# Performance work log

Measured on AMD Instinct MI355X. Metric: run time of the kernel, lower is better.

Reference implementation:

```python
import jax, jax.numpy as jnp
import numpy as np

N = 20000
NEG_SLOPE = 0.2
BN_EPS = 1e-5


def gat_layer(x, src, dst, W, a_src, a_dst, bias, heads, out_c, concat):
    # x: [N, in_c]; projection to [N, H, C]
    h = (x @ W).reshape(N, heads, out_c)
    al_s = jnp.einsum('nhc,hc->nh', h, a_src)   # per-node source logits
    al_d = jnp.einsum('nhc,hc->nh', h, a_dst)   # per-node dest logits
    e = al_s[src] + al_d[dst]                   # [E, H]
    e = jnp.where(e > 0, e, NEG_SLOPE * e)      # leaky_relu
    # segment softmax over incoming edges of each destination node
    emax = jax.ops.segment_max(e, dst, num_segments=N)
    ee = jnp.exp(e - emax[dst])
    denom = jax.ops.segment_sum(ee, dst, num_segments=N)
    alpha = ee / denom[dst]                     # [E, H]
    msg = h[src] * alpha[:, :, None]            # [E, H, C]
    out = jax.ops.segment_sum(msg, dst, num_segments=N)  # [N, H, C]
    out = out.reshape(N, heads * out_c) if concat else out.mean(axis=1)
    return out + bias


def batchnorm(x, gamma, beta):
    mu = x.mean(axis=0)
    var = x.var(axis=0)
    return (x - mu) * jax.lax.rsqrt(var + BN_EPS) * gamma + beta


def setup_inputs() -> dict:
    key = jax.random.key(0)
    ks = jax.random.split(key, 16)
    E = 320000
    in_c, hid, out_c, H = 128, 32, 16, 8

    def xavier(k, fan_in, fan_out):
        lim = np.sqrt(6.0 / (fan_in + fan_out))
        return jax.random.uniform(k, (fan_in, fan_out), jnp.float32, -lim, lim)

    x = jax.random.normal(ks[0], (N, in_c), jnp.float32)
    edge_index = jax.random.randint(ks[1], (2, E), 0, N, jnp.int32)
    d = {
        'x': x, 'edge_index': edge_index,
        'W0': xavier(ks[2], in_c, hid * H),
        'as0': jax.random.normal(ks[3], (H, hid), jnp.float32) * 0.1,
        'ad0': jax.random.normal(ks[4], (H, hid), jnp.float32) * 0.1,
        'b0': jnp.zeros((hid * H,), jnp.float32),
        'g0': jnp.ones((hid * H,), jnp.float32),
        'be0': jnp.zeros((hid * H,), jnp.float32),
        'W1': xavier(ks[5], hid * H, hid * H),
        'as1': jax.random.normal(ks[6], (H, hid), jnp.float32) * 0.1,
        'ad1': jax.random.normal(ks[7], (H, hid), jnp.float32) * 0.1,
        'b1': jnp.zeros((hid * H,), jnp.float32),
        'g1': jnp.ones((hid * H,), jnp.float32),
        'be1': jnp.zeros((hid * H,), jnp.float32),
        'W2': xavier(ks[8], hid * H, out_c),
        'as2': jax.random.normal(ks[9], (1, out_c), jnp.float32) * 0.1,
        'ad2': jax.random.normal(ks[10], (1, out_c), jnp.float32) * 0.1,
        'b2': jnp.zeros((out_c,), jnp.float32),
    }
    return d


def reference(x, edge_index, W0, as0, ad0, b0, g0, be0,
              W1, as1, ad1, b1, g1, be1, W2, as2, ad2, b2):
    # add self-loops (PyG GATConv default)
    loop = jnp.arange(N, dtype=edge_index.dtype)
    src = jnp.concatenate([edge_index[0], loop])
    dst = jnp.concatenate([edge_index[1], loop])

    h = gat_layer(x, src, dst, W0, as0, ad0, b0, heads=8, out_c=32, concat=True)
    h = jax.nn.relu(batchnorm(h, g0, be0))  # dropout inactive (eval)
    h = gat_layer(h, src, dst, W1, as1, ad1, b1, heads=8, out_c=32, concat=True)
    h = jax.nn.relu(batchnorm(h, g1, be1))
    h = gat_layer(h, src, dst, W2, as2, ad2, b2, heads=1, out_c=16, concat=False)
    return jax.nn.log_softmax(h, axis=-1)
```

## Files before the change

kernel.cpp:

```cpp
#include <hip/hip_runtime.h>
#include <hip/hip_bf16.h>
#include <math.h>


#define LRELU(v) ((v) > 0.f ? (v) : 0.2f * (v))
#define MAXDEG 128

typedef __attribute__((ext_vector_type(8))) short short8v;
typedef __attribute__((ext_vector_type(4))) float f32x4;

__device__ __forceinline__ unsigned short f2b(float f) {
    unsigned u = __float_as_uint(f);
    unsigned r = (u + 0x7fffu + ((u >> 16) & 1u)) >> 16;
    return (unsigned short)r;
}
__device__ __forceinline__ float bl(unsigned u) { return __uint_as_float(u << 16); }
__device__ __forceinline__ float bh(unsigned u) { return __uint_as_float(u & 0xffff0000u); }
__device__ __forceinline__ float b2f(unsigned short u) {
    return __uint_as_float((unsigned)u << 16);
}
__device__ __forceinline__ unsigned pack2(float a, float b) {
    return (unsigned)f2b(a) | ((unsigned)f2b(b) << 16);
}

__device__ __forceinline__ void cvt_body(const float* __restrict__ W,
                                         unsigned short* __restrict__ Wt,
                                         int IN, int OUT, int bx, int by,
                                         float* t ) {
    int tx = threadIdx.x & 31, ty = threadIdx.x >> 5;
    int c0 = bx * 32;
    int r0 = by * 32;
#pragma unroll
    for (int j = 0; j < 32; j += 8)
        t[(ty + j) * 33 + tx] = W[(size_t)(r0 + ty + j) * OUT + c0 + tx];
    __syncthreads();
#pragma unroll
    for (int j = 0; j < 32; j += 8)
        Wt[(size_t)(c0 + ty + j) * IN + r0 + tx] = f2b(t[tx * 33 + ty + j]);
}

__global__ void fill_cvt_k(unsigned* __restrict__ zp, int nz, int gF,
                           const float* __restrict__ W0,
                           unsigned short* __restrict__ Wt0,
                           const float* __restrict__ W1,
                           unsigned short* __restrict__ Wt1) {
    __shared__ float t[32 * 33];
    int b = blockIdx.x;
    if (b < gF) {
        int i = b * 256 + threadIdx.x;
        if (i < nz) zp[i] = 0u;
    } else {
        b -= gF;
        if (b < 32) cvt_body(W0, Wt0, 128, 256, b & 7, b >> 3, t);
        else { b -= 32; cvt_body(W1, Wt1, 256, 256, b & 7, b >> 3, t); }
    }
}

template <int IN, int MODE>
__device__ __forceinline__ void gemm_body(
        const void* __restrict__ Xv,
        const unsigned short* __restrict__ Wt,
        const float* __restrict__ as, const float* __restrict__ ad,
        unsigned short* __restrict__ Y,
        float* __restrict__ als, float* __restrict__ ald, int M,
        int bx, int by, unsigned short* Xs, unsigned short* Ws) {
    constexpr int LDT = 72;
    const int tid = threadIdx.x;
    const int lane = tid & 63, wid = tid >> 6;
    const int wr = wid >> 1, wc = wid & 1;
    const int cl = lane & 15, kg = lane >> 4;
    const int row0 = bx * 64, col0 = by * 64;
    const int sr = tid >> 3;
    const int sk = (tid & 7) * 8;

    f32x4 acc[2][2] = {};

    for (int k0 = 0; k0 < IN; k0 += 64) {
        uint4 xu0 = {0, 0, 0, 0}, xu1 = {0, 0, 0, 0};
        int xr0 = row0 + sr, xr1 = row0 + sr + 32;
        if (MODE == 0) {
            const float* Xf = (const float*)Xv;
            if (xr0 < M) {
                const float* p = Xf + (size_t)xr0 * IN + k0 + sk;
                float4 a = *(const float4*)p, b = *(const float4*)(p + 4);
                xu0 = make_uint4(pack2(a.x, a.y), pack2(a.z, a.w),
                                 pack2(b.x, b.y), pack2(b.z, b.w));
            }
            if (xr1 < M) {
                const float* p = Xf + (size_t)xr1 * IN + k0 + sk;
                float4 a = *(const float4*)p, b = *(const float4*)(p + 4);
                xu1 = make_uint4(pack2(a.x, a.y), pack2(a.z, a.w),
                                 pack2(b.x, b.y), pack2(b.z, b.w));
            }
        } else {
            const unsigned short* Xb = (const unsigned short*)Xv;
            if (xr0 < M) xu0 = *(const uint4*)&Xb[(size_t)xr0 * IN + k0 + sk];
            if (xr1 < M) xu1 = *(const uint4*)&Xb[(size_t)xr1 * IN + k0 + sk];
        }
        uint4 wv0 = *(const uint4*)&Wt[(size_t)(col0 + sr) * IN + k0 + sk];
        uint4 wv1 = *(const uint4*)&Wt[(size_t)(col0 + sr + 32) * IN + k0 + sk];
        __syncthreads();
        *(uint4*)&Xs[sr * LDT + sk] = xu0;
        *(uint4*)&Xs[(sr + 32) * LDT + sk] = xu1;
        *(uint4*)&Ws[sr * LDT + sk] = wv0;
        *(uint4*)&Ws[(sr + 32) * LDT + sk] = wv1;
        __syncthreads();
#pragma unroll
        for (int kk = 0; kk < 64; kk += 32) {
            const int ko = kk + kg * 8;
            short8v a0 = *(const short8v*)&Xs[(wr * 32 + cl) * LDT + ko];
            short8v a1 = *(const short8v*)&Xs[(wr * 32 + 16 + cl) * LDT + ko];
            short8v b0 = *(const short8v*)&Ws[(wc * 32 + cl) * LDT + ko];
            short8v b1 = *(const short8v*)&Ws[(wc * 32 + 16 + cl) * LDT + ko];
            acc[0][0] = __builtin_amdgcn_mfma_f32_16x16x32_bf16(a0, b0, acc[0][0], 0, 0, 0);
            acc[0][1] = __builtin_amdgcn_mfma_f32_16x16x32_bf16(a0, b1, acc[0][1], 0, 0, 0);
            acc[1][0] = __builtin_amdgcn_mfma_f32_16x16x32_bf16(a1, b0, acc[1][0], 0, 0, 0);
            acc[1][1] = __builtin_amdgcn_mfma_f32_16x16x32_bf16(a1, b1, acc[1][1], 0, 0, 0);
        }
    }

#pragma unroll
    for (int mt = 0; mt < 2; mt++)
#pragma unroll
        for (int j = 0; j < 4; j++) {
            int r = row0 + wr * 32 + mt * 16 + kg * 4 + j;
            if (r < M) {
#pragma unroll
                for (int nt = 0; nt < 2; nt++)
                    Y[(size_t)r * 256 + col0 + wc * 32 + nt * 16 + cl] =
                        f2b(acc[mt][nt][j]);
            }
        }

    const int h = 2 * by + wc;
    float as0v = as[h * 32 + cl], as1v = as[h * 32 + 16 + cl];
    float ad0v = ad[h * 32 + cl], ad1v = ad[h * 32 + 16 + cl];
#pragma unroll
    for (int mt = 0; mt < 2; mt++)
#pragma unroll
        for (int j = 0; j < 4; j++) {
            float ps = acc[mt][0][j] * as0v + acc[mt][1][j] * as1v;
            float pd = acc[mt][0][j] * ad0v + acc[mt][1][j] * ad1v;
            ps += __shfl_xor(ps, 1); ps += __shfl_xor(ps, 2);
            ps += __shfl_xor(ps, 4); ps += __shfl_xor(ps, 8);
            pd += __shfl_xor(pd, 1); pd += __shfl_xor(pd, 2);
            pd += __shfl_xor(pd, 4); pd += __shfl_xor(pd, 8);
            int r = row0 + wr * 32 + mt * 16 + kg * 4 + j;
            if (cl == 0 && r < M) {
                als[r * 8 + h] = ps;
                ald[r * 8 + h] = pd;
            }
        }
}

__global__ __launch_bounds__(256) void scatter_gemm0_k(
        const int* __restrict__ ei, int E, int N, int gE,
        int* __restrict__ cnt, int* __restrict__ ssrc,
        const float* __restrict__ x, const unsigned short* __restrict__ Wt0,
        const float* __restrict__ as0, const float* __restrict__ ad0,
        unsigned short* __restrict__ Y,
        float* __restrict__ als, float* __restrict__ ald) {
    __shared__ unsigned short Xs[64 * 72];
    __shared__ unsigned short Ws[64 * 72];
    int b = blockIdx.x;
    if (b < gE) {
        int e = b * 256 + threadIdx.x;
        if (e >= E + N) return;
        int s, d;
        if (e < E) { s = ei[e]; d = ei[E + e]; }
        else       { s = d = e - E; }
        int pos = atomicAdd(&cnt[d], 1);
        if (pos < MAXDEG) ssrc[(size_t)d * MAXDEG + pos] = s;
    } else {
        b -= gE;
        gemm_body<128, 0>(x, Wt0, as0, ad0, Y, als, ald, N, b >> 2, b & 3,
                          Xs, Ws);
    }
}

__global__ __launch_bounds__(256) void gemm_mfma1_k(
        const unsigned short* __restrict__ Xb,
        const unsigned short* __restrict__ Wt,
        const float* __restrict__ as, const float* __restrict__ ad,
        unsigned short* __restrict__ Y,
        float* __restrict__ als, float* __restrict__ ald, int M) {
    __shared__ unsigned short Xs[64 * 72];
    __shared__ unsigned short Ws[64 * 72];
    gemm_body<256, 1>(Xb, Wt, as, ad, Y, als, ald, M,
                      blockIdx.x, blockIdx.y, Xs, Ws);
}

template <int IN>
__global__ void gemm16_k(const unsigned short* __restrict__ X,
                         const float* __restrict__ W,
                         const float* __restrict__ as, const float* __restrict__ ad,
                         float* __restrict__ Y,
                         float* __restrict__ als, float* __restrict__ ald, int M) {
    constexpr int ROWS = 32, OUT = 16, RPT = 2;
    __shared__ float xs[ROWS][IN];
    const int row0 = blockIdx.x * ROWS;
    const int tid = threadIdx.x;
    for (int idx = tid; idx < ROWS * IN; idx += 256) {
        int r = idx / IN, k = idx % IN;
        int gr = row0 + r;
        xs[r][k] = (gr < M) ? b2f(X[(size_t)gr * IN + k]) : 0.f;
    }
    __syncthreads();
    const int j = tid & 15;
    const int rbase = (tid >> 4) * RPT;
    float acc[RPT] = {};
    for (int k = 0; k < IN; k++) {
        float w = W[k * OUT + j];
#pragma unroll
        for (int r = 0; r < RPT; r++) acc[r] += xs[rbase + r][k] * w;
    }
    float a1 = as[j], d1 = ad[j];
#pragma unroll
    for (int r = 0; r < RPT; r++) {
        int gr = row0 + rbase + r;
        if (gr < M) Y[gr * OUT + j] = acc[r];
        float ps = acc[r] * a1, pd = acc[r] * d1;
#pragma unroll
        for (int off = 8; off; off >>= 1) {
            ps += __shfl_xor(ps, off, 16);
            pd += __shfl_xor(pd, off, 16);
        }
        if (j == 0 && gr < M) { als[gr] = ps; ald[gr] = pd; }
    }
}

__global__ void agg8_csr_k(const int* __restrict__ cnt,
                           const int* __restrict__ ssrc,
                           const float* __restrict__ als,
                           const float* __restrict__ ald,
                           const unsigned short* __restrict__ feat,
                           const float* __restrict__ bias,
                           unsigned short* __restrict__ aggb, int N) {
    int lane = threadIdx.x & 63;
    int n = blockIdx.x * 4 + (threadIdx.x >> 6);
    if (n >= N) return;
    int len = cnt[n];
    if (len > MAXDEG) len = MAXDEG;
    const size_t base = (size_t)n * MAXDEG;
    const int grp = lane >> 4;
    const int l = lane & 15;
    const int h = l >> 1;
    const int c0 = l * 16;
    const float adh = ald[n * 8 + h];

    float acc[16] = {};
    float den = 0.f;
    for (int e = grp; e < len; e += 4) {
        int s = ssrc[base + e];
        float v = als[s * 8 + h] + adh;
        v = LRELU(v);
        float p = __expf(v);
        den += p;
        const unsigned short* fp = feat + (size_t)s * 256 + c0;
        uint4 f0 = *(const uint4*)fp;
        uint4 f1 = *(const uint4*)(fp + 8);
        acc[0]  += bl(f0.x) * p; acc[1]  += bh(f0.x) * p;
        acc[2]  += bl(f0.y) * p; acc[3]  += bh(f0.y) * p;
        acc[4]  += bl(f0.z) * p; acc[5]  += bh(f0.z) * p;
        acc[6]  += bl(f0.w) * p; acc[7]  += bh(f0.w) * p;
        acc[8]  += bl(f1.x) * p; acc[9]  += bh(f1.x) * p;
        acc[10] += bl(f1.y) * p; acc[11] += bh(f1.y) * p;
        acc[12] += bl(f1.z) * p; acc[13] += bh(f1.z) * p;
        acc[14] += bl(f1.w) * p; acc[15] += bh(f1.w) * p;
    }
    den += __shfl_xor(den, 16); den += __shfl_xor(den, 32);
#pragma unroll
    for (int j = 0; j < 16; j++) {
        acc[j] += __shfl_xor(acc[j], 16);
        acc[j] += __shfl_xor(acc[j], 32);
    }
    if (lane < 16) {
        float inv = 1.f / den;
        float4 ba = *(const float4*)(bias + c0);
        float4 bb = *(const float4*)(bias + c0 + 4);
        float4 bc = *(const float4*)(bias + c0 + 8);
        float4 bd = *(const float4*)(bias + c0 + 12);
        uint4 o0, o1;
        o0.x = pack2(acc[0]  * inv + ba.x, acc[1]  * inv + ba.y);
        o0.y = pack2(acc[2]  * inv + ba.z, acc[3]  * inv + ba.w);
        o0.z = pack2(acc[4]  * inv + bb.x, acc[5]  * inv + bb.y);
        o0.w = pack2(acc[6]  * inv + bb.z, acc[7]  * inv + bb.w);
        o1.x = pack2(acc[8]  * inv + bc.x, acc[9]  * inv + bc.y);
        o1.y = pack2(acc[10] * inv + bc.z, acc[11] * inv + bc.w);
        o1.z = pack2(acc[12] * inv + bd.x, acc[13] * inv + bd.y);
        o1.w = pack2(acc[14] * inv + bd.z, acc[15] * inv + bd.w);
        unsigned short* op = aggb + (size_t)n * 256 + c0;
        *(uint4*)op = o0;
        *(uint4*)(op + 8) = o1;
    }
}

__global__ void agg1_ls_k(const int* __restrict__ cnt,
                          const int* __restrict__ ssrc,
                          const float* __restrict__ als,
                          const float* __restrict__ ald,
                          const float* __restrict__ feat,
                          const float* __restrict__ b2,
                          float* __restrict__ out, int N) {
    int lane = threadIdx.x & 63;
    int n = blockIdx.x * 4 + (threadIdx.x >> 6);
    if (n >= N) return;
    int len = cnt[n];
    if (len > MAXDEG) len = MAXDEG;
    const size_t base = (size_t)n * MAXDEG;
    float adh = ald[n];

    int slot = lane >> 4, c = lane & 15;
    float acc = 0.f, den = 0.f;
    for (int e = slot; e < len; e += 4) {
        int s = ssrc[base + e];
        float v = als[s] + adh;
        v = LRELU(v);
        float p = __expf(v);
        den += p;
        acc += feat[s * 16 + c] * p;
    }
    acc += __shfl_xor(acc, 16); acc += __shfl_xor(acc, 32);
    den += __shfl_xor(den, 16); den += __shfl_xor(den, 32);

    float v = acc / den + b2[c];
    float mm = v;
#pragma unroll
    for (int off = 8; off; off >>= 1) mm = fmaxf(mm, __shfl_xor(mm, off, 16));
    float ex = __expf(v - mm);
    float ssum = ex;
#pragma unroll
    for (int off = 8; off; off >>= 1) ssum += __shfl_xor(ssum, off, 16);
    if (lane < 16) out[n * 16 + c] = v - mm - logf(ssum);
}

__global__ void bn_stats_k(const unsigned short* __restrict__ agg,
                           float* __restrict__ stats, int N) {
    __shared__ float red[2][8][256];
    const int t = threadIdx.x;
    const int ch0 = (t & 31) * 8;
    const int rslot = t >> 5;
    const int chunk = (N + 63) >> 6;
    const int r0 = blockIdx.x * chunk;
    int r1 = r0 + chunk; if (r1 > N) r1 = N;
    float s[8] = {}, q[8] = {};
    for (int r = r0 + rslot; r < r1; r += 8) {
        uint4 u = *(const uint4*)(agg + (size_t)r * 256 + ch0);
        float v;
        v = bl(u.x); s[0] += v; q[0] += v * v;
        v = bh(u.x); s[1] += v; q[1] += v * v;
        v = bl(u.y); s[2] += v; q[2] += v * v;
        v = bh(u.y); s[3] += v; q[3] += v * v;
        v = bl(u.z); s[4] += v; q[4] += v * v;
        v = bh(u.z); s[5] += v; q[5] += v * v;
        v = bl(u.w); s[6] += v; q[6] += v * v;
        v = bh(u.w); s[7] += v; q[7] += v * v;
    }
#pragma unroll
    for (int j = 0; j < 8; j++) {
        red[0][rslot][ch0 + j] = s[j];
        red[1][rslot][ch0 + j] = q[j];
    }
    __syncthreads();
    float ss = 0.f, qq = 0.f;
#pragma unroll
    for (int k = 0; k < 8; k++) {
        ss += red[0][k][t];
        qq += red[1][k][t];
    }
    atomicAdd(&stats[t], ss);
    atomicAdd(&stats[256 + t], qq);
}

__global__ void bn_apply_k(const unsigned short* __restrict__ agg,
                           const float* __restrict__ stats,
                           const float* __restrict__ g,
                           const float* __restrict__ be,
                           unsigned short* __restrict__ outp, int N) {
    int gid = blockIdx.x * 256 + threadIdx.x;
    if (gid >= N * 64) return;
    int c = (gid & 63) * 4;
    float invN = 1.f / (float)N;
    uint2 u = *(const uint2*)(agg + (size_t)gid * 4);
    float v[4] = {bl(u.x), bh(u.x), bl(u.y), bh(u.y)};
    unsigned ow[2];
#pragma unroll
    for (int j = 0; j < 2; j++) {
        unsigned lo = 0, hi = 0;
#pragma unroll
        for (int k = 0; k < 2; k++) {
            int ch = c + j * 2 + k;
            float mu = stats[ch] * invN;
            float var = stats[256 + ch] * invN - mu * mu;
            float o = (v[j * 2 + k] - mu) * rsqrtf(var + 1e-5f) * g[ch] + be[ch];
            o = o > 0.f ? o : 0.f;
            if (k == 0) lo = f2b(o); else hi = f2b(o);
        }
        ow[j] = lo | (hi << 16);
    }
    *(uint2*)(outp + (size_t)gid * 4) = make_uint2(ow[0], ow[1]);
}

extern "C" void kernel_launch(void* const* d_in, const int* in_sizes, int n_in,
                              void* d_out, int out_size, void* d_ws, size_t ws_size,
                              hipStream_t stream) {
    const float* x   = (const float*)d_in[0];
    const int*   ei  = (const int*)d_in[1];
    const float* W0  = (const float*)d_in[2];
    const float* as0 = (const float*)d_in[3];
    const float* ad0 = (const float*)d_in[4];
    const float* b0  = (const float*)d_in[5];
    const float* g0  = (const float*)d_in[6];
    const float* be0 = (const float*)d_in[7];
    const float* W1  = (const float*)d_in[8];
    const float* as1 = (const float*)d_in[9];
    const float* ad1 = (const float*)d_in[10];
    const float* b1  = (const float*)d_in[11];
    const float* g1  = (const float*)d_in[12];
    const float* be1 = (const float*)d_in[13];
    const float* W2  = (const float*)d_in[14];
    const float* as2 = (const float*)d_in[15];
    const float* ad2 = (const float*)d_in[16];
    const float* b2  = (const float*)d_in[17];
    float* out = (float*)d_out;

    const int N = in_sizes[0] / 128;
    const int E = in_sizes[1] / 2;
    const int ET = E + N;

    float* ws = (float*)d_ws;
    size_t o = 0;
    int* cnt    = (int*)(ws + o); o += (size_t)N;
    float* stats0 = ws + o; o += 512;
    float* stats1 = ws + o; o += 512;
    unsigned short* bufA = (unsigned short*)(ws + o); o += (size_t)N * 128;
    unsigned short* bufB = (unsigned short*)(ws + o); o += (size_t)N * 128;
    unsigned short* Wt0  = (unsigned short*)(ws + o); o += 256 * 128 / 2;
    unsigned short* Wt1  = (unsigned short*)(ws + o); o += 256 * 256 / 2;
    float* als  = ws + o;  o += (size_t)N * 8;
    float* ald  = ws + o;  o += (size_t)N * 8;
    float* h2   = ws + o;  o += (size_t)N * 16;
    float* als2 = ws + o;  o += (size_t)N;
    float* ald2 = ws + o;  o += (size_t)N;
    int* ssrc   = (int*)(ws + o); o += (size_t)N * MAXDEG;

    const int gE    = (ET + 255) / 256;
    const int gF    = (N + 1024 + 255) / 256;
    const int gApply = (N * 64 + 255) / 256;
    const int gWave = (N + 3) / 4;
    const int gGemmN = ((N + 63) / 64) * 4;

    fill_cvt_k<<<gF + 96, 256, 0, stream>>>((unsigned*)cnt, N + 1024, gF,
                                            W0, Wt0, W1, Wt1);
    scatter_gemm0_k<<<gE + gGemmN, 256, 0, stream>>>(ei, E, N, gE, cnt, ssrc,
                                                     x, Wt0, as0, ad0, bufA,
                                                     als, ald);

    agg8_csr_k<<<gWave, 256, 0, stream>>>(cnt, ssrc, als, ald, bufA, b0,
                                          bufB, N);
    bn_stats_k<<<64, 256, 0, stream>>>(bufB, stats0, N);
    bn_apply_k<<<gApply, 256, 0, stream>>>(bufB, stats0, g0, be0, bufA, N);

    gemm_mfma1_k<<<dim3((N + 63) / 64, 4), 256, 0, stream>>>(bufA, Wt1, as1,
                                                             ad1, bufB, als,
                                                             ald, N);
    agg8_csr_k<<<gWave, 256, 0, stream>>>(cnt, ssrc, als, ald, bufB, b1,
                                          bufA, N);
    bn_stats_k<<<64, 256, 0, stream>>>(bufA, stats1, N);
    bn_apply_k<<<gApply, 256, 0, stream>>>(bufA, stats1, g1, be1, bufB, N);

    gemm16_k<256><<<(N + 31) / 32, 256, 0, stream>>>(bufB, W2, as2, ad2, h2,
                                                     als2, ald2, N);
    agg1_ls_k<<<gWave, 256, 0, stream>>>(cnt, ssrc, als2, ald2, h2, b2, out, N);
}
```

Measured before the change: 186.1 us.

## Store CSR source indices as 16-bit and widen per-lane head slices in aggregation

Source-node indices in the padded CSR are now stored as unsigned short instead of int, halving index bytes written by the scatter and read by both aggregation kernels (N=20000 fits in 16 bits). The 8-head aggregation kernel is remapped so each lane handles one head with 32 channels and 8 edge groups run in parallel, instead of 16 channels and 4 groups. This cuts index traffic and issues more edges concurrently per wave, at the cost of doubled accumulator registers and an extra shuffle-reduction stage. The 16-bit index silently breaks for graphs with more than 65535 nodes.

```diff
diff --git a/kernel.cpp b/kernel.cpp
--- a/kernel.cpp
+++ b/kernel.cpp
@@ -155,7 +155,7 @@
 
 __global__ __launch_bounds__(256) void scatter_gemm0_k(
         const int* __restrict__ ei, int E, int N, int gE,
-        int* __restrict__ cnt, int* __restrict__ ssrc,
+        int* __restrict__ cnt, unsigned short* __restrict__ ssrc,
         const float* __restrict__ x, const unsigned short* __restrict__ Wt0,
         const float* __restrict__ as0, const float* __restrict__ ad0,
         unsigned short* __restrict__ Y,
@@ -170,7 +170,7 @@
         if (e < E) { s = ei[e]; d = ei[E + e]; }
         else       { s = d = e - E; }
         int pos = atomicAdd(&cnt[d], 1);
-        if (pos < MAXDEG) ssrc[(size_t)d * MAXDEG + pos] = s;
+        if (pos < MAXDEG) ssrc[(size_t)d * MAXDEG + pos] = (unsigned short)s;
     } else {
         b -= gE;
         gemm_body<128, 0>(x, Wt0, as0, ad0, Y, als, ald, N, b >> 2, b & 3,
@@ -230,7 +230,7 @@
 }
 
 __global__ void agg8_csr_k(const int* __restrict__ cnt,
-                           const int* __restrict__ ssrc,
+                           const unsigned short* __restrict__ ssrc,
                            const float* __restrict__ als,
                            const float* __restrict__ ald,
                            const unsigned short* __restrict__ feat,
@@ -242,16 +242,15 @@
     int len = cnt[n];
     if (len > MAXDEG) len = MAXDEG;
     const size_t base = (size_t)n * MAXDEG;
-    const int grp = lane >> 4;
-    const int l = lane & 15;
-    const int h = l >> 1;
-    const int c0 = l * 16;
+    const int grp = lane >> 3;
+    const int h = lane & 7;
+    const int c0 = h * 32;
     const float adh = ald[n * 8 + h];
 
-    float acc[16] = {};
+    float acc[32] = {};
     float den = 0.f;
-    for (int e = grp; e < len; e += 4) {
-        int s = ssrc[base + e];
+    for (int e = grp; e < len; e += 8) {
+        int s = (int)ssrc[base + e];
         float v = als[s * 8 + h] + adh;
         v = LRELU(v);
         float p = __expf(v);
@@ -259,6 +258,8 @@
         const unsigned short* fp = feat + (size_t)s * 256 + c0;
         uint4 f0 = *(const uint4*)fp;
         uint4 f1 = *(const uint4*)(fp + 8);
+        uint4 f2 = *(const uint4*)(fp + 16);
+        uint4 f3 = *(const uint4*)(fp + 24);
         acc[0]  += bl(f0.x) * p; acc[1]  += bh(f0.x) * p;
         acc[2]  += bl(f0.y) * p; acc[3]  += bh(f0.y) * p;
         acc[4]  += bl(f0.z) * p; acc[5]  += bh(f0.z) * p;
@@ -267,36 +268,41 @@
         acc[10] += bl(f1.y) * p; acc[11] += bh(f1.y) * p;
         acc[12] += bl(f1.z) * p; acc[13] += bh(f1.z) * p;
         acc[14] += bl(f1.w) * p; acc[15] += bh(f1.w) * p;
-    }
-    den += __shfl_xor(den, 16); den += __shfl_xor(den, 32);
-#pragma unroll
-    for (int j = 0; j < 16; j++) {
+        acc[16] += bl(f2.x) * p; acc[17] += bh(f2.x) * p;
+        acc[18] += bl(f2.y) * p; acc[19] += bh(f2.y) * p;
+        acc[20] += bl(f2.z) * p; acc[21] += bh(f2.z) * p;
+        acc[22] += bl(f2.w) * p; acc[23] += bh(f2.w) * p;
+        acc[24] += bl(f3.x) * p; acc[25] += bh(f3.x) * p;
+        acc[26] += bl(f3.y) * p; acc[27] += bh(f3.y) * p;
+        acc[28] += bl(f3.z) * p; acc[29] += bh(f3.z) * p;
+        acc[30] += bl(f3.w) * p; acc[31] += bh(f3.w) * p;
+    }
+    den += __shfl_xor(den, 8); den += __shfl_xor(den, 16); den += __shfl_xor(den, 32);
+#pragma unroll
+    for (int j = 0; j < 32; j++) {
+        acc[j] += __shfl_xor(acc[j], 8);
         acc[j] += __shfl_xor(acc[j], 16);
         acc[j] += __shfl_xor(acc[j], 32);
     }
-    if (lane < 16) {
+    if (lane < 8) {
         float inv = 1.f / den;
-        float4 ba = *(const float4*)(bias + c0);
-        float4 bb = *(const float4*)(bias + c0 + 4);
-        float4 bc = *(const float4*)(bias + c0 + 8);
-        float4 bd = *(const float4*)(bias + c0 + 12);
-        uint4 o0, o1;
-        o0.x = pack2(acc[0]  * inv + ba.x, acc[1]  * inv + ba.y);
-        o0.y = pack2(acc[2]  * inv + ba.z, acc[3]  * inv + ba.w);
-        o0.z = pack2(acc[4]  * inv + bb.x, acc[5]  * inv + bb.y);
-        o0.w = pack2(acc[6]  * inv + bb.z, acc[7]  * inv + bb.w);
-        o1.x = pack2(acc[8]  * inv + bc.x, acc[9]  * inv + bc.y);
-        o1.y = pack2(acc[10] * inv + bc.z, acc[11] * inv + bc.w);
-        o1.z = pack2(acc[12] * inv + bd.x, acc[13] * inv + bd.y);
-        o1.w = pack2(acc[14] * inv + bd.z, acc[15] * inv + bd.w);
         unsigned short* op = aggb + (size_t)n * 256 + c0;
-        *(uint4*)op = o0;
-        *(uint4*)(op + 8) = o1;
+#pragma unroll
+        for (int q = 0; q < 4; q++) {
+            float4 b4a = *(const float4*)(bias + c0 + q * 8);
+            float4 b4b = *(const float4*)(bias + c0 + q * 8 + 4);
+            uint4 ov;
+            ov.x = pack2(acc[q * 8 + 0] * inv + b4a.x, acc[q * 8 + 1] * inv + b4a.y);
+            ov.y = pack2(acc[q * 8 + 2] * inv + b4a.z, acc[q * 8 + 3] * inv + b4a.w);
+            ov.z = pack2(acc[q * 8 + 4] * inv + b4b.x, acc[q * 8 + 5] * inv + b4b.y);
+            ov.w = pack2(acc[q * 8 + 6] * inv + b4b.z, acc[q * 8 + 7] * inv + b4b.w);
+            *(uint4*)(op + q * 8) = ov;
+        }
     }
 }
 
 __global__ void agg1_ls_k(const int* __restrict__ cnt,
-                          const int* __restrict__ ssrc,
+                          const unsigned short* __restrict__ ssrc,
                           const float* __restrict__ als,
                           const float* __restrict__ ald,
                           const float* __restrict__ feat,
@@ -313,7 +319,7 @@
     int slot = lane >> 4, c = lane & 15;
     float acc = 0.f, den = 0.f;
     for (int e = slot; e < len; e += 4) {
-        int s = ssrc[base + e];
+        int s = (int)ssrc[base + e];
         float v = als[s] + adh;
         v = LRELU(v);
         float p = __expf(v);
@@ -442,7 +448,7 @@
     float* h2   = ws + o;  o += (size_t)N * 16;
     float* als2 = ws + o;  o += (size_t)N;
     float* ald2 = ws + o;  o += (size_t)N;
-    int* ssrc   = (int*)(ws + o); o += (size_t)N * MAXDEG;
+    unsigned short* ssrc = (unsigned short*)(ws + o); o += (size_t)N * MAXDEG / 2;
 
     const int gE    = (ET + 255) / 256;
     const int gF    = (N + 1024 + 255) / 256;
```

Result: slower. 197.7 us (+6.2%).
